# Performance work log

Measured on AMD Instinct MI355X. Metric: run time of the kernel, lower is better.

## Reference

```python
import jax, jax.numpy as jnp
import numpy as np

V = 10000      # vocabulary_size
T = 20         # max_len
D = 512        # D_img == hidden size
H = 64         # actor/critic hidden
FI = 2048      # image feature dim
FB = 256       # box feature dim (FI + FB == 2304)
B = 1024       # batch
N_WORDS = 50   # allowed word_list size


def setup_inputs() -> dict:
    key = jax.random.key(0)
    ks = iter(jax.random.split(key, 40))
    def p(shape, s=0.02):
        return (jax.random.normal(next(ks), shape) * s).astype(jnp.float32)
    z = lambda *s: jnp.zeros(s, jnp.float32)
    inp = {
        "image_feature": jax.random.normal(next(ks), (B, FI), dtype=jnp.float32),
        "box_feature": jax.random.normal(next(ks), (B, FB), dtype=jnp.float32),
        # feature_resizer Linear(2304, D)
        "fr_w": p((FI + FB, D)), "fr_b": z(D),
        # _block dense1 / dense2 (each: Linear(D,D), GELU, Linear(D,D))
        "d1a_w": p((D, D)), "d1a_b": z(D), "d1b_w": p((D, D)), "d1b_b": z(D),
        "d2a_w": p((D, D)), "d2a_b": z(D), "d2b_w": p((D, D)), "d2b_b": z(D),
        # encoder LayerNorm (affine) + Linear(D, 512)
        "ln_g": jnp.ones((D,), jnp.float32), "ln_b": z(D),
        "eo_w": p((D, 512)), "eo_b": z(512),
        # word embedding
        "emb": p((V, 512)),
        # GRUCell weights, torch gate order (r, z, n)
        "gwi": p((512, 3 * 512)), "gwh": p((512, 3 * 512)),
        "gbi": z(3 * 512), "gbh": z(3 * 512),
        # actor: 512->64 tanh 64->64 tanh 64->V
        "a1_w": p((512, H)), "a1_b": z(H),
        "a2_w": p((H, H)), "a2_b": z(H),
        "a3_w": p((H, V), 0.01), "a3_b": z(V),
        # critic: 512->64 tanh 64->64 tanh 64->1
        "c1_w": p((512, H)), "c1_b": z(H),
        "c2_w": p((H, H)), "c2_b": z(H),
        "c3_w": p((H, 1)), "c3_b": z(1),
        # frozen word mask: 0 for allowed words, -1000 otherwise
        "word_mask": jnp.where(jnp.arange(V) < N_WORDS, 0.0, -1000.0).astype(jnp.float32),
    }
    return inp


def _ln(x, g=None, b=None):
    m = x.mean(-1, keepdims=True)
    v = x.var(-1, keepdims=True)
    y = (x - m) * jax.lax.rsqrt(v + 1e-5)
    return y if g is None else y * g + b


def _forward(image_feature, box_feature, fr_w, fr_b,
             d1a_w, d1a_b, d1b_w, d1b_b, d2a_w, d2a_b, d2b_w, d2b_b,
             ln_g, ln_b, eo_w, eo_b, emb, gwi, gwh, gbi, gbh,
             a1_w, a1_b, a2_w, a2_b, a3_w, a3_b,
             c1_w, c1_b, c2_w, c2_b, c3_w, c3_b, word_mask):
    gelu = lambda t: jax.nn.gelu(t, approximate=False)
    # feature resizer + residual block + LN + projection (encoder)
    x0 = jnp.concatenate([image_feature, box_feature], axis=1) @ fr_w + fr_b
    y = gelu(_ln(x0) @ d1a_w + d1a_b) @ d1b_w + d1b_b
    y = _ln(y + x0)
    x = x0 + (gelu(y @ d2a_w + d2a_b) @ d2b_w + d2b_b)
    img = _ln(x, ln_g, ln_b) @ eo_w + eo_b          # [B, 512]

    samp_key = jax.random.key(1)

    def step(carry, t):
        hx, ix = carry
        # torch: hx = GRUCell(input=hx, hidden=ix)
        gi = hx @ gwi + gbi
        gh = ix @ gwh + gbh
        gir, giz, gin = jnp.split(gi, 3, axis=-1)
        ghr, ghz, ghn = jnp.split(gh, 3, axis=-1)
        r = jax.nn.sigmoid(gir + ghr)
        zg = jax.nn.sigmoid(giz + ghz)
        n = jnp.tanh(gin + r * ghn)
        h = (1.0 - zg) * n + zg * ix                # new hidden [B, 512]
        logits = jnp.tanh(jnp.tanh(h @ a1_w + a1_b) @ a2_w + a2_b) @ a3_w + a3_b + word_mask
        logp = jax.nn.log_softmax(logits, axis=-1)  # [B, V]
        act = jax.random.categorical(jax.random.fold_in(samp_key, t), logp, axis=-1)  # [B]
        lp = jnp.take_along_axis(logp, act[:, None], axis=-1)[:, 0]
        ent = -jnp.sum(jnp.exp(logp) * logp, axis=-1)
        val = (jnp.tanh(jnp.tanh(h @ c1_w + c1_b) @ c2_w + c2_b) @ c3_w + c3_b)[:, 0]
        return (h, emb[act]), (act, lp, ent, val)

    _, (acts, lps, ents, vals) = jax.lax.scan(step, (img, jnp.zeros_like(img)), jnp.arange(T))
    # scan stacks along time first -> transpose to [B, T]
    return acts.T, lps.T, ents.T, vals.T[..., None]


def reference(image_feature, box_feature, fr_w, fr_b,
              d1a_w, d1a_b, d1b_w, d1b_b, d2a_w, d2a_b, d2b_w, d2b_b,
              ln_g, ln_b, eo_w, eo_b, emb, gwi, gwh, gbi, gbh,
              a1_w, a1_b, a2_w, a2_b, a3_w, a3_b,
              c1_w, c1_b, c2_w, c2_b, c3_w, c3_b, word_mask):
    return _forward(image_feature, box_feature, fr_w, fr_b,
                    d1a_w, d1a_b, d1b_w, d1b_b, d2a_w, d2a_b, d2b_w, d2b_b,
                    ln_g, ln_b, eo_w, eo_b, emb, gwi, gwh, gbi, gbh,
                    a1_w, a1_b, a2_w, a2_b, a3_w, a3_b,
                    c1_w, c1_b, c2_w, c2_b, c3_w, c3_b, word_mask)
```

## Files before the change

kernel.cpp:

```cpp
#include <hip/hip_runtime.h>
#include <math.h>
#include <stdint.h>

#define BB 1024
#define DD 512
#define VV 10000
#define TT 20
#define NW 50

__host__ __device__ __forceinline__ void tf2x32(uint32_t k0, uint32_t k1,
                                                uint32_t x0, uint32_t x1,
                                                uint32_t& o0, uint32_t& o1) {
  uint32_t ks2 = k0 ^ k1 ^ 0x1BD11BDAu;
  x0 += k0; x1 += k1;
#define ROTL(x,r) (((x)<<(r))|((x)>>(32-(r))))
#define RND(r) { x0 += x1; x1 = ROTL(x1,(r)); x1 ^= x0; }
  RND(13) RND(15) RND(26) RND(6)   x0 += k1;  x1 += ks2 + 1u;
  RND(17) RND(29) RND(16) RND(24)  x0 += ks2; x1 += k0 + 2u;
  RND(13) RND(15) RND(26) RND(6)   x0 += k0;  x1 += k1 + 3u;
  RND(17) RND(29) RND(16) RND(24)  x0 += k1;  x1 += ks2 + 4u;
  RND(13) RND(15) RND(26) RND(6)   x0 += ks2; x1 += k0 + 5u;
#undef RND
#undef ROTL
  o0 = x0; o1 = x1;
}

__device__ __forceinline__ float wave_sum(float v) {
#pragma unroll
  for (int o = 32; o > 0; o >>= 1) v += __shfl_xor(v, o, 64);
  return v;
}
__device__ __forceinline__ float wave_max(float v) {
#pragma unroll
  for (int o = 32; o > 0; o >>= 1) v = fmaxf(v, __shfl_xor(v, o, 64));
  return v;
}

__device__ __forceinline__ float gelu_f(float x) {
  float u = x / 1.4142135623730951f;
  float e = (float)erf((double)u);
  return x * (e + 1.0f) * 0.5f;
}

template<int ACT, bool RES, bool CONCAT>
__device__ __forceinline__ void gemm_body(
    const float* __restrict__ A, const float* __restrict__ A2, int K1,
    const float* __restrict__ W, int ldw, const float* __restrict__ bias,
    const float* __restrict__ res, float* __restrict__ C, int N, int K)
{
  __shared__ alignas(16) float As[32][68];
  __shared__ alignas(16) float Ws[32][68];
  const int bm = blockIdx.x * 64;
  const int bn = blockIdx.y * 64;
  const int tid = threadIdx.x;
  const int tr = (tid >> 4) << 2;
  const int tc = (tid & 15) << 2;
  const int am = tid & 63;
  const int ak = (tid >> 6) << 3;
  const int wr = tid >> 3;
  const int wc = (tid & 7) << 3;
  float acc[4][4] = {};
  for (int k0 = 0; k0 < K; k0 += 32) {
    {
      const int row = bm + am;
#pragma unroll
      for (int h = 0; h < 2; h++) {
        int gk = k0 + ak + 4 * h;
        float4 v;
        if (CONCAT) {
          v = (gk < K1) ? *(const float4*)&A[(size_t)row * K1 + gk]
                        : *(const float4*)&A2[(size_t)row * (K - K1) + (gk - K1)];
        } else {
          v = *(const float4*)&A[(size_t)row * K + gk];
        }
        int kb = ak + 4 * h;
        As[kb + 0][am] = v.x; As[kb + 1][am] = v.y;
        As[kb + 2][am] = v.z; As[kb + 3][am] = v.w;
      }
    }
    {
      const float* wsrc = &W[(size_t)(k0 + wr) * ldw + bn + wc];
      *(float4*)&Ws[wr][wc]     = *(const float4*)(wsrc);
      *(float4*)&Ws[wr][wc + 4] = *(const float4*)(wsrc + 4);
    }
    __syncthreads();
#pragma unroll
    for (int kk = 0; kk < 32; kk++) {
      float4 av = *(const float4*)&As[kk][tr];
      float4 bv = *(const float4*)&Ws[kk][tc];
      acc[0][0] = fmaf(av.x, bv.x, acc[0][0]);
      acc[0][1] = fmaf(av.x, bv.y, acc[0][1]);
      acc[0][2] = fmaf(av.x, bv.z, acc[0][2]);
      acc[0][3] = fmaf(av.x, bv.w, acc[0][3]);
      acc[1][0] = fmaf(av.y, bv.x, acc[1][0]);
      acc[1][1] = fmaf(av.y, bv.y, acc[1][1]);
      acc[1][2] = fmaf(av.y, bv.z, acc[1][2]);
      acc[1][3] = fmaf(av.y, bv.w, acc[1][3]);
      acc[2][0] = fmaf(av.z, bv.x, acc[2][0]);
      acc[2][1] = fmaf(av.z, bv.y, acc[2][1]);
      acc[2][2] = fmaf(av.z, bv.z, acc[2][2]);
      acc[2][3] = fmaf(av.z, bv.w, acc[2][3]);
      acc[3][0] = fmaf(av.w, bv.x, acc[3][0]);
      acc[3][1] = fmaf(av.w, bv.y, acc[3][1]);
      acc[3][2] = fmaf(av.w, bv.z, acc[3][2]);
      acc[3][3] = fmaf(av.w, bv.w, acc[3][3]);
    }
    __syncthreads();
  }
#pragma unroll
  for (int i = 0; i < 4; i++) {
    int m = bm + tr + i;
#pragma unroll
    for (int j = 0; j < 4; j++) {
      int n = bn + tc + j;
      float v = acc[i][j] + bias[n];
      if (ACT == 1) v = gelu_f(v);
      if (RES) v = v + res[(size_t)m * N + n];
      C[(size_t)m * N + n] = v;
    }
  }
}

template<int ACT, bool RES, bool CONCAT>
__global__ __launch_bounds__(256) void sgemm_k(
    const float* __restrict__ A, const float* __restrict__ A2, int K1,
    const float* __restrict__ W, int ldw, const float* __restrict__ bias,
    const float* __restrict__ res, float* __restrict__ C, int N, int K)
{
  gemm_body<ACT, RES, CONCAT>(A, A2, K1, W, ldw, bias, res, C, N, K);
}

template<bool AFFINE, bool ADD>
__global__ __launch_bounds__(256) void lnorm_k(
    const float* __restrict__ X, const float* __restrict__ X2,
    const float* __restrict__ g, const float* __restrict__ bt,
    float* __restrict__ Y)
{
  __shared__ float red[8];
  int row = blockIdx.x, tid = threadIdx.x;
  const float* x = X + (size_t)row * DD;
  float v0 = x[tid], v1 = x[tid + 256];
  if (ADD) {
    const float* x2 = X2 + (size_t)row * DD;
    v0 += x2[tid]; v1 += x2[tid + 256];
  }
  float s = wave_sum(v0 + v1);
  if ((tid & 63) == 0) red[tid >> 6] = s;
  __syncthreads();
  float mean = (red[0] + red[1] + red[2] + red[3]) * (1.0f / 512.0f);
  float d0 = v0 - mean, d1 = v1 - mean;
  float s2 = wave_sum(d0 * d0 + d1 * d1);
  if ((tid & 63) == 0) red[4 + (tid >> 6)] = s2;
  __syncthreads();
  float var = (red[4] + red[5] + red[6] + red[7]) * (1.0f / 512.0f);
  float rs = (float)(1.0 / sqrt((double)(var + 1e-5f)));
  float y0 = d0 * rs, y1 = d1 * rs;
  if (AFFINE) {
    y0 = y0 * g[tid] + bt[tid];
    y1 = y1 * g[tid + 256] + bt[tid + 256];
  }
  Y[(size_t)row * DD + tid] = y0;
  Y[(size_t)row * DD + tid + 256] = y1;
}

__global__ __launch_bounds__(256) void gru_pw2(
    const float* __restrict__ gi, const float* __restrict__ table,
    const float* __restrict__ gbh, const float* __restrict__ emb,
    const float* __restrict__ out, int t, float* __restrict__ hx)
{
  int idx = blockIdx.x * 256 + threadIdx.x;
  int b = idx >> 9, j = idx & 511;
  const float* ghb;
  float ixv;
  if (t == 0) {
    ghb = gbh;
    ixv = 0.f;
  } else {
    int a = (int)out[(size_t)b * TT + (t - 1)];
    ghb = table + (size_t)a * 1536;
    ixv = emb[(size_t)a * DD + j];
  }
  const float* gib = gi + (size_t)b * 1536;
  float r = (float)(1.0 / (1.0 + exp(-(double)(gib[j] + ghb[j]))));
  float z = (float)(1.0 / (1.0 + exp(-(double)(gib[DD + j] + ghb[DD + j]))));
  float narg = gib[2 * DD + j] + r * ghb[2 * DD + j];
  float n = (float)tanh((double)narg);
  hx[idx] = (1.0f - z) * n + z * ixv;
}

__global__ __launch_bounds__(64) void head_sample(
    const float* __restrict__ hx,
    const float* __restrict__ a1w, const float* __restrict__ a1b,
    const float* __restrict__ a2w, const float* __restrict__ a2b,
    const float* __restrict__ a3w, const float* __restrict__ a3b,
    const float* __restrict__ c1w, const float* __restrict__ c1b,
    const float* __restrict__ c2w, const float* __restrict__ c2b,
    const float* __restrict__ c3w, const float* __restrict__ c3b,
    const float* __restrict__ wmask,
    float* __restrict__ out,
    int t, uint32_t fk0, uint32_t fk1)
{
  int b = blockIdx.x;
  int lane = threadIdx.x;
  __shared__ float sh[DD];
  __shared__ float st1[64], st2[64], sc1[64];
  const float* hr = hx + (size_t)b * DD;
  for (int i = lane; i < DD; i += 64) sh[i] = hr[i];
  __syncthreads();

  float aa0 = 0, aa1 = 0, aa2 = 0, aa3 = 0, ca0 = 0, ca1 = 0, ca2 = 0, ca3 = 0;
  for (int k = 0; k < DD; k += 4) {
    float h0 = sh[k], h1 = sh[k + 1], h2 = sh[k + 2], h3 = sh[k + 3];
    aa0 = fmaf(h0, a1w[(k + 0) * 64 + lane], aa0);
    aa1 = fmaf(h1, a1w[(k + 1) * 64 + lane], aa1);
    aa2 = fmaf(h2, a1w[(k + 2) * 64 + lane], aa2);
    aa3 = fmaf(h3, a1w[(k + 3) * 64 + lane], aa3);
    ca0 = fmaf(h0, c1w[(k + 0) * 64 + lane], ca0);
    ca1 = fmaf(h1, c1w[(k + 1) * 64 + lane], ca1);
    ca2 = fmaf(h2, c1w[(k + 2) * 64 + lane], ca2);
    ca3 = fmaf(h3, c1w[(k + 3) * 64 + lane], ca3);
  }
  st1[lane] = (float)tanh((double)(((aa0 + aa1) + (aa2 + aa3)) + a1b[lane]));
  sc1[lane] = (float)tanh((double)(((ca0 + ca1) + (ca2 + ca3)) + c1b[lane]));
  __syncthreads();

  float a2acc = 0, c2acc = 0;
  for (int k = 0; k < 64; k++) {
    a2acc = fmaf(st1[k], a2w[k * 64 + lane], a2acc);
    c2acc = fmaf(sc1[k], c2w[k * 64 + lane], c2acc);
  }
  st2[lane] = (float)tanh((double)(a2acc + a2b[lane]));
  float t2c = (float)tanh((double)(c2acc + c2b[lane]));
  __syncthreads();

  float val = wave_sum(t2c * c3w[lane]) + c3b[0];

  float lg = -INFINITY;
  if (lane < NW) {
    float s = 0;
    for (int k = 0; k < 64; k++) s = fmaf(st2[k], a3w[k * VV + lane], s);
    lg = (s + a3b[lane]) + wmask[lane];
  }

  float m = wave_max(lg);
  float shf = 0.f, e = 0.f;
  if (lane < NW) { shf = lg - m; e = (float)exp((double)shf); }
  float se = wave_sum(e);
  float lse = (float)log((double)se);
  float logp = shf - lse;
  float term = 0.f;
  if (lane < NW) { float p = (float)exp((double)logp); term = p * logp; }
  float ent = -wave_sum(term);

  float score = -INFINITY;
  if (lane < NW) {
    uint32_t i = (uint32_t)b * (uint32_t)VV + (uint32_t)lane;
    uint32_t o0, o1;
    tf2x32(fk0, fk1, 0u, i, o0, o1);
    uint32_t bits = o0 ^ o1;
    uint32_t mant = bits >> 9;
    float u = (mant == 0u) ? 1.17549435e-38f
                           : (float)mant * 1.1920928955078125e-7f;
    float l1 = (float)log((double)u);
    float l2 = (float)log((double)(-l1));
    score = -l2 + logp;
  }

  float best = score; int bi = lane;
#pragma unroll
  for (int off = 32; off > 0; off >>= 1) {
    float ob = __shfl_xor(best, off, 64);
    int oi = __shfl_xor(bi, off, 64);
    if (ob > best || (ob == best && oi < bi)) { best = ob; bi = oi; }
  }
  float lp = __shfl(logp, bi, 64);

  if (lane == 0) {
    out[(size_t)b * TT + t] = (float)bi;
    out[(size_t)BB * TT + (size_t)b * TT + t] = lp;
    out[2 * (size_t)BB * TT + (size_t)b * TT + t] = ent;
    out[3 * (size_t)BB * TT + (size_t)b * TT + t] = val;
  }
}

__global__ __launch_bounds__(256) void diag_k(float* out, float code, int n) {
  int i = blockIdx.x * 256 + threadIdx.x;
  if (i < n) out[i] = code;
}

extern "C" void kernel_launch(void* const* d_in, const int* in_sizes, int n_in,
                              void* d_out, int out_size, void* d_ws, size_t ws_size,
                              hipStream_t stream) {
  static const int EXP_SIZES[34] = {
    2097152, 262144, 1179648, 512, 262144, 512, 262144, 512, 262144, 512,
    262144, 512, 512, 512, 262144, 512, 5120000, 786432, 786432, 1536,
    1536, 32768, 64, 4096, 64, 640000, 10000, 32768, 64, 4096,
    64, 64, 1, 10000 };
  double code = 0.0;
  if (n_in != 34) code = 1e6 + (double)n_in;
  else {
    for (int i = 0; i < 34; i++)
      if (in_sizes[i] != EXP_SIZES[i]) { code = 2e6 + i * 1e4 + (in_sizes[i] % 10000); break; }
  }
  if (code == 0.0 && out_size != 4 * BB * TT) code = 3e6 + (double)(out_size % 1000000);
  if (code == 0.0 && ws_size < (size_t)24 * 1024 * 1024) {
    size_t kb = ws_size / 1024; if (kb > 999999) kb = 999999;
    code = 4e6 + (double)kb;
  }
  if (code != 0.0) {
    diag_k<<<(out_size + 255) / 256, 256, 0, stream>>>((float*)d_out, (float)code, out_size);
    return;
  }

  const float* image = (const float*)d_in[0];
  const float* boxf  = (const float*)d_in[1];
  const float* fr_w  = (const float*)d_in[2];
  const float* fr_b  = (const float*)d_in[3];
  const float* d1a_w = (const float*)d_in[4];
  const float* d1a_b = (const float*)d_in[5];
  const float* d1b_w = (const float*)d_in[6];
  const float* d1b_b = (const float*)d_in[7];
  const float* d2a_w = (const float*)d_in[8];
  const float* d2a_b = (const float*)d_in[9];
  const float* d2b_w = (const float*)d_in[10];
  const float* d2b_b = (const float*)d_in[11];
  const float* ln_g  = (const float*)d_in[12];
  const float* ln_b  = (const float*)d_in[13];
  const float* eo_w  = (const float*)d_in[14];
  const float* eo_b  = (const float*)d_in[15];
  const float* emb   = (const float*)d_in[16];
  const float* gwi   = (const float*)d_in[17];
  const float* gwh   = (const float*)d_in[18];
  const float* gbi   = (const float*)d_in[19];
  const float* gbh   = (const float*)d_in[20];
  const float* a1w   = (const float*)d_in[21];
  const float* a1b   = (const float*)d_in[22];
  const float* a2w   = (const float*)d_in[23];
  const float* a2b   = (const float*)d_in[24];
  const float* a3w   = (const float*)d_in[25];
  const float* a3b   = (const float*)d_in[26];
  const float* c1w   = (const float*)d_in[27];
  const float* c1b   = (const float*)d_in[28];
  const float* c2w   = (const float*)d_in[29];
  const float* c2b   = (const float*)d_in[30];
  const float* c3w   = (const float*)d_in[31];
  const float* c3b   = (const float*)d_in[32];
  const float* wmask = (const float*)d_in[33];

  float* ws = (float*)d_ws;
  const size_t R = (size_t)BB * DD;
  float* hx    = ws;
  float* gi    = ws + R;
  float* table = ws + 4 * R;
  float* P = gi;
  float* Q = gi + R;
  float* S = gi + 2 * R;
  float* U = ws + 4 * R + 2 * R;
  float* out = (float*)d_out;

  dim3 blk(256);
  sgemm_k<0, false, false><<<dim3(1, 24), blk, 0, stream>>>(emb, nullptr, 0, gwh, 1536, gbh, nullptr, table, 1536, 512);
  sgemm_k<0, false, true><<<dim3(16, 8), blk, 0, stream>>>(image, boxf, 2048, fr_w, 512, fr_b, nullptr, P, 512, 2304);
  lnorm_k<false, false><<<BB, blk, 0, stream>>>(P, nullptr, nullptr, nullptr, Q);
  sgemm_k<1, false, false><<<dim3(16, 8), blk, 0, stream>>>(Q, nullptr, 0, d1a_w, 512, d1a_b, nullptr, S, 512, 512);
  sgemm_k<0, false, false><<<dim3(16, 8), blk, 0, stream>>>(S, nullptr, 0, d1b_w, 512, d1b_b, nullptr, U, 512, 512);
  lnorm_k<false, true><<<BB, blk, 0, stream>>>(U, P, nullptr, nullptr, Q);
  sgemm_k<1, false, false><<<dim3(16, 8), blk, 0, stream>>>(Q, nullptr, 0, d2a_w, 512, d2a_b, nullptr, S, 512, 512);
  sgemm_k<0, true, false><<<dim3(16, 8), blk, 0, stream>>>(S, nullptr, 0, d2b_w, 512, d2b_b, P, U, 512, 512);
  lnorm_k<true, false><<<BB, blk, 0, stream>>>(U, nullptr, ln_g, ln_b, Q);
  sgemm_k<0, false, false><<<dim3(16, 8), blk, 0, stream>>>(Q, nullptr, 0, eo_w, 512, eo_b, nullptr, hx, 512, 512);

  for (int t = 0; t < TT; t++) {
    uint32_t fk0, fk1;
    tf2x32(0u, 1u, 0u, (uint32_t)t, fk0, fk1);
    sgemm_k<0, false, false><<<dim3(16, 24), blk, 0, stream>>>(hx, nullptr, 0, gwi, 1536, gbi, nullptr, gi, 1536, 512);
    gru_pw2<<<2048, blk, 0, stream>>>(gi, table, gbh, emb, out, t, hx);
    head_sample<<<BB, dim3(64), 0, stream>>>(hx, a1w, a1b, a2w, a2b, a3w, a3b,
                                             c1w, c1b, c2w, c2b, c3w, c3b,
                                             wmask, out, t, fk0, fk1);
  }
}
```

Before: 1.652 ms.

## Fuse GRU pointwise into head kernel and retile GEMM to single-wave prefetched tiles

Replaces the 256-thread 64x64 SGEMM with a 64-thread 32x32 tile kernel that prefetches the next K tile into registers and writes output as float4. Launches four times as many blocks so the small GEMMs fill more CUs. Fuses the GRU gate pointwise step into the per-row head/sample kernel, so each step drops one launch and one round-trip of hx through global memory. Smaller tiles mean less reuse per loaded element and more blocks in total.

```diff
diff --git a/kernel.cpp b/kernel.cpp
--- a/kernel.cpp
+++ b/kernel.cpp
@@ -43,47 +43,52 @@
 }
 
 template<int ACT, bool RES, bool CONCAT>
-__device__ __forceinline__ void gemm_body(
+__global__ __launch_bounds__(64) void wgemm_k(
     const float* __restrict__ A, const float* __restrict__ A2, int K1,
     const float* __restrict__ W, int ldw, const float* __restrict__ bias,
     const float* __restrict__ res, float* __restrict__ C, int N, int K)
 {
-  __shared__ alignas(16) float As[32][68];
-  __shared__ alignas(16) float Ws[32][68];
-  const int bm = blockIdx.x * 64;
-  const int bn = blockIdx.y * 64;
-  const int tid = threadIdx.x;
-  const int tr = (tid >> 4) << 2;
-  const int tc = (tid & 15) << 2;
-  const int am = tid & 63;
-  const int ak = (tid >> 6) << 3;
-  const int wr = tid >> 3;
-  const int wc = (tid & 7) << 3;
+  __shared__ alignas(16) float As[32][40];
+  __shared__ alignas(16) float Ws[32][40];
+  const int bm = blockIdx.x * 32;
+  const int bn = blockIdx.y * 32;
+  const int lane = threadIdx.x;
+  const int tr = (lane >> 3) << 2;
+  const int tc = (lane & 7) << 2;
+  const int am  = lane & 31;
+  const int ak0 = (lane >> 5) << 2;
+  const int wr0 = lane >> 3;
+  const int wc  = (lane & 7) << 2;
+
+  float4 pa[4], pw[4];
+  auto load_tile = [&](int k0) {
+#pragma unroll
+    for (int h = 0; h < 4; h++) {
+      int kq = ak0 + 8 * h;
+      int gk = k0 + kq;
+      if (CONCAT) {
+        pa[h] = (gk < K1) ? *(const float4*)&A[(size_t)(bm + am) * K1 + gk]
+                          : *(const float4*)&A2[(size_t)(bm + am) * (K - K1) + (gk - K1)];
+      } else {
+        pa[h] = *(const float4*)&A[(size_t)(bm + am) * K + gk];
+      }
+      int wr = wr0 + 8 * h;
+      pw[h] = *(const float4*)&W[(size_t)(k0 + wr) * ldw + bn + wc];
+    }
+  };
+
   float acc[4][4] = {};
+  load_tile(0);
   for (int k0 = 0; k0 < K; k0 += 32) {
-    {
-      const int row = bm + am;
-#pragma unroll
-      for (int h = 0; h < 2; h++) {
-        int gk = k0 + ak + 4 * h;
-        float4 v;
-        if (CONCAT) {
-          v = (gk < K1) ? *(const float4*)&A[(size_t)row * K1 + gk]
-                        : *(const float4*)&A2[(size_t)row * (K - K1) + (gk - K1)];
-        } else {
-          v = *(const float4*)&A[(size_t)row * K + gk];
-        }
-        int kb = ak + 4 * h;
-        As[kb + 0][am] = v.x; As[kb + 1][am] = v.y;
-        As[kb + 2][am] = v.z; As[kb + 3][am] = v.w;
-      }
-    }
-    {
-      const float* wsrc = &W[(size_t)(k0 + wr) * ldw + bn + wc];
-      *(float4*)&Ws[wr][wc]     = *(const float4*)(wsrc);
-      *(float4*)&Ws[wr][wc + 4] = *(const float4*)(wsrc + 4);
+#pragma unroll
+    for (int h = 0; h < 4; h++) {
+      int kq = ak0 + 8 * h;
+      As[kq + 0][am] = pa[h].x; As[kq + 1][am] = pa[h].y;
+      As[kq + 2][am] = pa[h].z; As[kq + 3][am] = pa[h].w;
+      *(float4*)&Ws[wr0 + 8 * h][wc] = pw[h];
     }
     __syncthreads();
+    if (k0 + 32 < K) load_tile(k0 + 32);
 #pragma unroll
     for (int kk = 0; kk < 32; kk++) {
       float4 av = *(const float4*)&As[kk][tr];
@@ -110,24 +115,18 @@
 #pragma unroll
   for (int i = 0; i < 4; i++) {
     int m = bm + tr + i;
+    float4 o;
+    float* op = (float*)&o;
 #pragma unroll
     for (int j = 0; j < 4; j++) {
       int n = bn + tc + j;
       float v = acc[i][j] + bias[n];
       if (ACT == 1) v = gelu_f(v);
       if (RES) v = v + res[(size_t)m * N + n];
-      C[(size_t)m * N + n] = v;
+      op[j] = v;
     }
-  }
-}
-
-template<int ACT, bool RES, bool CONCAT>
-__global__ __launch_bounds__(256) void sgemm_k(
-    const float* __restrict__ A, const float* __restrict__ A2, int K1,
-    const float* __restrict__ W, int ldw, const float* __restrict__ bias,
-    const float* __restrict__ res, float* __restrict__ C, int N, int K)
-{
-  gemm_body<ACT, RES, CONCAT>(A, A2, K1, W, ldw, bias, res, C, N, K);
+    *(float4*)&C[(size_t)m * N + bn + tc] = o;
+  }
 }
 
 template<bool AFFINE, bool ADD>
@@ -163,33 +162,9 @@
   Y[(size_t)row * DD + tid + 256] = y1;
 }
 
-__global__ __launch_bounds__(256) void gru_pw2(
+__global__ __launch_bounds__(64) void gru_head(
     const float* __restrict__ gi, const float* __restrict__ table,
     const float* __restrict__ gbh, const float* __restrict__ emb,
-    const float* __restrict__ out, int t, float* __restrict__ hx)
-{
-  int idx = blockIdx.x * 256 + threadIdx.x;
-  int b = idx >> 9, j = idx & 511;
-  const float* ghb;
-  float ixv;
-  if (t == 0) {
-    ghb = gbh;
-    ixv = 0.f;
-  } else {
-    int a = (int)out[(size_t)b * TT + (t - 1)];
-    ghb = table + (size_t)a * 1536;
-    ixv = emb[(size_t)a * DD + j];
-  }
-  const float* gib = gi + (size_t)b * 1536;
-  float r = (float)(1.0 / (1.0 + exp(-(double)(gib[j] + ghb[j]))));
-  float z = (float)(1.0 / (1.0 + exp(-(double)(gib[DD + j] + ghb[DD + j]))));
-  float narg = gib[2 * DD + j] + r * ghb[2 * DD + j];
-  float n = (float)tanh((double)narg);
-  hx[idx] = (1.0f - z) * n + z * ixv;
-}
-
-__global__ __launch_bounds__(64) void head_sample(
-    const float* __restrict__ hx,
     const float* __restrict__ a1w, const float* __restrict__ a1b,
     const float* __restrict__ a2w, const float* __restrict__ a2b,
     const float* __restrict__ a3w, const float* __restrict__ a3b,
@@ -197,15 +172,30 @@
     const float* __restrict__ c2w, const float* __restrict__ c2b,
     const float* __restrict__ c3w, const float* __restrict__ c3b,
     const float* __restrict__ wmask,
-    float* __restrict__ out,
+    float* __restrict__ hx, float* __restrict__ out,
     int t, uint32_t fk0, uint32_t fk1)
 {
   int b = blockIdx.x;
   int lane = threadIdx.x;
   __shared__ float sh[DD];
   __shared__ float st1[64], st2[64], sc1[64];
-  const float* hr = hx + (size_t)b * DD;
-  for (int i = lane; i < DD; i += 64) sh[i] = hr[i];
+
+  int a = (t > 0) ? (int)out[(size_t)b * TT + (t - 1)] : -1;
+  const float* ghb = (a >= 0) ? (table + (size_t)a * 1536) : gbh;
+  const float* gib = gi + (size_t)b * 1536;
+  const float* er  = (a >= 0) ? (emb + (size_t)a * DD) : nullptr;
+#pragma unroll
+  for (int jj = 0; jj < 8; jj++) {
+    int j = lane + 64 * jj;
+    float ixv = (a >= 0) ? er[j] : 0.f;
+    float r = (float)(1.0 / (1.0 + exp(-(double)(gib[j] + ghb[j]))));
+    float z = (float)(1.0 / (1.0 + exp(-(double)(gib[DD + j] + ghb[DD + j]))));
+    float narg = gib[2 * DD + j] + r * ghb[2 * DD + j];
+    float n = (float)tanh((double)narg);
+    float h = (1.0f - z) * n + z * ixv;
+    sh[j] = h;
+    hx[(size_t)b * DD + j] = h;
+  }
   __syncthreads();
 
   float aa0 = 0, aa1 = 0, aa2 = 0, aa3 = 0, ca0 = 0, ca1 = 0, ca2 = 0, ca3 = 0;
@@ -351,32 +341,32 @@
   const size_t R = (size_t)BB * DD;
   float* hx    = ws;
   float* gi    = ws + R;
-  float* table = ws + 4 * R;
-  float* P = gi;
-  float* Q = gi + R;
-  float* S = gi + 2 * R;
-  float* U = ws + 4 * R + 2 * R;
+  float* Q     = ws + 4 * R;
+  float* S     = ws + 5 * R;
+  float* U     = ws + 6 * R;
+  float* table = ws + 7 * R;
+  float* P     = gi;
   float* out = (float*)d_out;
 
-  dim3 blk(256);
-  sgemm_k<0, false, false><<<dim3(1, 24), blk, 0, stream>>>(emb, nullptr, 0, gwh, 1536, gbh, nullptr, table, 1536, 512);
-  sgemm_k<0, false, true><<<dim3(16, 8), blk, 0, stream>>>(image, boxf, 2048, fr_w, 512, fr_b, nullptr, P, 512, 2304);
-  lnorm_k<false, false><<<BB, blk, 0, stream>>>(P, nullptr, nullptr, nullptr, Q);
-  sgemm_k<1, false, false><<<dim3(16, 8), blk, 0, stream>>>(Q, nullptr, 0, d1a_w, 512, d1a_b, nullptr, S, 512, 512);
-  sgemm_k<0, false, false><<<dim3(16, 8), blk, 0, stream>>>(S, nullptr, 0, d1b_w, 512, d1b_b, nullptr, U, 512, 512);
-  lnorm_k<false, true><<<BB, blk, 0, stream>>>(U, P, nullptr, nullptr, Q);
-  sgemm_k<1, false, false><<<dim3(16, 8), blk, 0, stream>>>(Q, nullptr, 0, d2a_w, 512, d2a_b, nullptr, S, 512, 512);
-  sgemm_k<0, true, false><<<dim3(16, 8), blk, 0, stream>>>(S, nullptr, 0, d2b_w, 512, d2b_b, P, U, 512, 512);
-  lnorm_k<true, false><<<BB, blk, 0, stream>>>(U, nullptr, ln_g, ln_b, Q);
-  sgemm_k<0, false, false><<<dim3(16, 8), blk, 0, stream>>>(Q, nullptr, 0, eo_w, 512, eo_b, nullptr, hx, 512, 512);
+  dim3 wblk(64);
+  wgemm_k<0, false, false><<<dim3(2, 48), wblk, 0, stream>>>(emb, nullptr, 0, gwh, 1536, gbh, nullptr, table, 1536, 512);
+  wgemm_k<0, false, true><<<dim3(32, 16), wblk, 0, stream>>>(image, boxf, 2048, fr_w, 512, fr_b, nullptr, P, 512, 2304);
+  lnorm_k<false, false><<<BB, dim3(256), 0, stream>>>(P, nullptr, nullptr, nullptr, Q);
+  wgemm_k<1, false, false><<<dim3(32, 16), wblk, 0, stream>>>(Q, nullptr, 0, d1a_w, 512, d1a_b, nullptr, S, 512, 512);
+  wgemm_k<0, false, false><<<dim3(32, 16), wblk, 0, stream>>>(S, nullptr, 0, d1b_w, 512, d1b_b, nullptr, U, 512, 512);
+  lnorm_k<false, true><<<BB, dim3(256), 0, stream>>>(U, P, nullptr, nullptr, Q);
+  wgemm_k<1, false, false><<<dim3(32, 16), wblk, 0, stream>>>(Q, nullptr, 0, d2a_w, 512, d2a_b, nullptr, S, 512, 512);
+  wgemm_k<0, true, false><<<dim3(32, 16), wblk, 0, stream>>>(S, nullptr, 0, d2b_w, 512, d2b_b, P, U, 512, 512);
+  lnorm_k<true, false><<<BB, dim3(256), 0, stream>>>(U, nullptr, ln_g, ln_b, Q);
+  wgemm_k<0, false, false><<<dim3(32, 16), wblk, 0, stream>>>(Q, nullptr, 0, eo_w, 512, eo_b, nullptr, hx, 512, 512);
 
   for (int t = 0; t < TT; t++) {
     uint32_t fk0, fk1;
     tf2x32(0u, 1u, 0u, (uint32_t)t, fk0, fk1);
-    sgemm_k<0, false, false><<<dim3(16, 24), blk, 0, stream>>>(hx, nullptr, 0, gwi, 1536, gbi, nullptr, gi, 1536, 512);
-    gru_pw2<<<2048, blk, 0, stream>>>(gi, table, gbh, emb, out, t, hx);
-    head_sample<<<BB, dim3(64), 0, stream>>>(hx, a1w, a1b, a2w, a2b, a3w, a3b,
-                                             c1w, c1b, c2w, c2b, c3w, c3b,
-                                             wmask, out, t, fk0, fk1);
-  }
-}
+    wgemm_k<0, false, false><<<dim3(32, 48), wblk, 0, stream>>>(hx, nullptr, 0, gwi, 1536, gbi, nullptr, gi, 1536, 512);
+    gru_head<<<BB, wblk, 0, stream>>>(gi, table, gbh, emb,
+                                      a1w, a1b, a2w, a2b, a3w, a3b,
+                                      c1w, c1b, c2w, c2b, c3w, c3b,
+                                      wmask, hx, out, t, fk0, fk1);
+  }
+}
```

Result: slower. 1.730 ms (+4.7%).
